# Kernel optimization log

Hardware: AMD Instinct MI355X
Metric: run time of the kernel (lower is better)

The kernel has to match this reference:

```python
import jax, jax.numpy as jnp
import numpy as np

CONFUSED_PAIRS = [(1, 2), (3, 4), (5, 6)]
NUM_CLASSES = 13
MARGIN = 0.5
IGNORE_INDEX = -100
BIG = 1e9  # finite sentinel instead of +/-inf (keeps grads clean)
EPS = 1e-12  # matches F.normalize eps

_conf_np = np.zeros((NUM_CLASSES, NUM_CLASSES), dtype=bool)
for _a, _b in CONFUSED_PAIRS:
    _conf_np[_a, _b] = True
    _conf_np[_b, _a] = True
CONF = jnp.asarray(_conf_np)  # [C, C] symmetric confused-class table


def setup_inputs() -> dict:
    key = jax.random.key(0)
    k1, k2 = jax.random.split(key)
    embeddings = jax.random.normal(k1, (16, 512, 256), dtype=jnp.float32)
    labels = jax.random.randint(k2, (16, 512), 0, 13, dtype=jnp.int64)
    return {"embeddings": embeddings, "labels": labels}


def reference(embeddings, labels):
    B, S, H = embeddings.shape
    e = embeddings.reshape(-1, H)                      # [N, H]
    lab = labels.reshape(-1)                           # [N]
    N = e.shape[0]

    valid = lab != IGNORE_INDEX                        # [N]
    # L2 normalize (F.normalize: divide by norm clamped to eps)
    norm = jnp.linalg.norm(e, axis=1, keepdims=True)
    e = e / jnp.maximum(norm, EPS)

    sim = e @ e.T                                      # [N, N] cosine sims

    lab_c = jnp.clip(lab, 0, NUM_CLASSES - 1)          # safe gather index
    # anchor label participates in some confused pair, and anchor is valid
    anchor_ok = valid & CONF[lab_c].any(axis=1)        # [N]

    same = lab[:, None] == lab[None, :]                # [N, N]
    eye = jnp.eye(N, dtype=bool)
    pos_mask = same & valid[None, :] & ~eye            # positives: same class, not self
    neg_mask = CONF[lab_c[:, None], lab_c[None, :]] & valid[None, :]  # confused-class negatives

    has_pos = pos_mask.any(axis=1)
    has_neg = neg_mask.any(axis=1)
    count_mask = anchor_ok & has_pos & has_neg         # [N] anchors contributing a triplet

    hardest_pos = jnp.min(jnp.where(pos_mask, sim, BIG), axis=1)   # [N]
    hardest_neg = jnp.max(jnp.where(neg_mask, sim, -BIG), axis=1)  # [N]

    triplet = jax.nn.relu(MARGIN + hardest_neg - hardest_pos)
    triplet = jnp.where(count_mask, triplet, 0.0)

    num_triplets = count_mask.sum()
    loss = triplet.sum() / jnp.maximum(num_triplets, 1).astype(triplet.dtype)
    return jnp.where(num_triplets > 0, loss, 0.0)
```

## Files before the change

### kernel.cpp

```cpp
#include <hip/hip_runtime.h>
#include <math.h>

#define Hdim    256
#define NMAX    8192
#define NPADMAX (NMAX + 6 * 32)
#define WLMAX   264
#define BIGV    1e9f
#define MARGIN  0.5f

typedef __attribute__((ext_vector_type(8))) short bf16x8;
typedef __attribute__((ext_vector_type(4))) float f32x4;

struct WS {
    unsigned short ebf[NPADMAX][Hdim];
    int gpos[NMAX];
    int S[8];
    int n[8];
    int wl_a[WLMAX];
    int wl_c[WLMAX];
    int T;
    unsigned done;
    float wsum;
    int   wcnt;
};

__device__ inline unsigned short f2bf(float f) {
    unsigned u = __float_as_uint(f);
    return (unsigned short)((u + 0x7fffu + ((u >> 16) & 1u)) >> 16);
}

__global__ __launch_bounds__(1024) void plan_kernel(const int* __restrict__ lab,
                                                    WS* ws, int N) {
    __shared__ int h[8];
    __shared__ int S[8];
    __shared__ int cur[8];
    const int tid = threadIdx.x;
    if (tid < 8) h[tid] = 0;
    __syncthreads();
    for (int i = tid; i < N; i += 1024) {
        int l = lab[i];
        if (l >= 1 && l <= 6) atomicAdd(&h[l], 1);
    }
    __syncthreads();
    if (tid == 0) {
        int acc = 0;
        for (int c = 1; c <= 6; ++c) { S[c] = acc; acc += ((h[c] + 31) >> 5) << 5; }
        S[0] = 0; S[7] = acc;
        int T = 0;
        for (int c = 1; c <= 6; ++c) {
            int nt = (h[c] + 31) >> 5;
            for (int k = 0; k < nt; ++k) { ws->wl_a[T] = S[c] + 32 * k; ws->wl_c[T] = c; ++T; }
        }
        ws->T = T;
        ws->done = 0u; ws->wsum = 0.f; ws->wcnt = 0;
        for (int c = 0; c < 8; ++c) { ws->n[c] = h[c]; ws->S[c] = S[c]; }
    }
    __syncthreads();
    if (tid < 8) cur[tid] = S[tid];
    __syncthreads();
    for (int i = tid; i < N; i += 1024) {
        int l = lab[i];
        ws->gpos[i] = (l >= 1 && l <= 6) ? atomicAdd(&cur[l], 1) : -1;
    }
}

__global__ __launch_bounds__(256) void norm_gather_kernel(const float* __restrict__ in,
                                                          WS* ws) {
    int row  = blockIdx.x * 4 + (threadIdx.x >> 6);
    int lane = threadIdx.x & 63;
    int g = ws->gpos[row];
    if (g < 0) return;
    float4 v = ((const float4*)(in + (size_t)row * Hdim))[lane];
    float ss = v.x*v.x + v.y*v.y + v.z*v.z + v.w*v.w;
    #pragma unroll
    for (int off = 32; off >= 1; off >>= 1) ss += __shfl_xor(ss, off);
    float sc = 1.0f / fmaxf(sqrtf(ss), 1e-12f);
    ushort4 o;
    o.x = f2bf(v.x * sc); o.y = f2bf(v.y * sc);
    o.z = f2bf(v.z * sc); o.w = f2bf(v.w * sc);
    ((ushort4*)(&ws->ebf[g][0]))[lane] = o;
}

__global__ __launch_bounds__(256) void sim_kernel(WS* ws, float* __restrict__ out) {
    const int wave = threadIdx.x >> 6;
    const int lane = threadIdx.x & 63;
    const int col  = lane & 15;
    const int quad = lane >> 4;
    const int tileIdx = blockIdx.x;

    __shared__ float lds_hp[4][32], lds_hn[4][32];

    if (tileIdx < ws->T) {
        const int aBase = ws->wl_a[tileIdx];
        const int c     = ws->wl_c[tileIdx];
        const int p     = ((c - 1) ^ 1) + 1;
        const int posS = ws->S[c], posRealE = posS + ws->n[c];
        const int negS = ws->S[p], negRealE = negS + ws->n[p];
        const int nPosT = (ws->S[c + 1] - posS) >> 4;
        const int nNegT = (ws->S[p + 1] - negS) >> 4;
        const int nTT   = nPosT + nNegT;
        const bool hasPN = (ws->n[c] >= 2) && (ws->n[p] >= 1);

        const unsigned short* ebf = &ws->ebf[0][0];

        bf16x8 afrag[2][8];
        #pragma unroll
        for (int t2 = 0; t2 < 2; ++t2) {
            const unsigned short* rp = ebf + (size_t)(aBase + t2 * 16 + col) * Hdim + quad * 8;
            #pragma unroll
            for (int ks = 0; ks < 8; ++ks)
                afrag[t2][ks] = *(const bf16x8*)(rp + ks * 32);
        }

        float runMin[2][4], runMax[2][4];
        #pragma unroll
        for (int t2 = 0; t2 < 2; ++t2)
            #pragma unroll
            for (int r = 0; r < 4; ++r) { runMin[t2][r] = BIGV; runMax[t2][r] = -BIGV; }

        auto j0Of = [&](int t) -> int {
            return (t < nPosT) ? (posS + (t << 4)) : (negS + ((t - nPosT) << 4));
        };
        bf16x8 b0[8], b1[8];
        auto loadB = [&](bf16x8 (&bf)[8], int t) {
            const unsigned short* rp = ebf + (size_t)(j0Of(t) + col) * Hdim + quad * 8;
            #pragma unroll
            for (int ks = 0; ks < 8; ++ks)
                bf[ks] = *(const bf16x8*)(rp + ks * 32);
        };
        auto computeT = [&](bf16x8 (&bf)[8], int t) {
            int j0 = j0Of(t);
            bool isPos = t < nPosT;
            int realE  = isPos ? posRealE : negRealE;
            bool valid = (j0 + col) < realE;
            #pragma unroll
            for (int t2 = 0; t2 < 2; ++t2) {
                f32x4 acc = {0.f, 0.f, 0.f, 0.f};
                #pragma unroll
                for (int ks = 0; ks < 8; ++ks)
                    acc = __builtin_amdgcn_mfma_f32_16x16x32_bf16(afrag[t2][ks], bf[ks], acc, 0, 0, 0);
                if (isPos) {
                    #pragma unroll
                    for (int r = 0; r < 4; ++r)
                        runMin[t2][r] = fminf(runMin[t2][r], valid ? acc[r] : BIGV);
                } else {
                    #pragma unroll
                    for (int r = 0; r < 4; ++r)
                        runMax[t2][r] = fmaxf(runMax[t2][r], valid ? acc[r] : -BIGV);
                }
            }
        };

        int nIter = (nTT > wave) ? ((nTT - wave + 3) >> 2) : 0;
        int t = wave, i = 0;
        if (nIter > 0) loadB(b0, t);
        while (i + 2 <= nIter) {
            loadB(b1, t + 4);
            computeT(b0, t);
            if (i + 2 < nIter) loadB(b0, t + 8);
            computeT(b1, t + 4);
            t += 8; i += 2;
        }
        if (i < nIter) computeT(b0, t);

        #pragma unroll
        for (int t2 = 0; t2 < 2; ++t2)
            #pragma unroll
            for (int r = 0; r < 4; ++r) {
                float mn = runMin[t2][r], mx = runMax[t2][r];
                #pragma unroll
                for (int off = 1; off < 16; off <<= 1) {
                    mn = fminf(mn, __shfl_xor(mn, off));
                    mx = fmaxf(mx, __shfl_xor(mx, off));
                }
                if (col == 0) {
                    int a = t2 * 16 + quad * 4 + r;
                    lds_hp[wave][a] = mn;
                    lds_hn[wave][a] = mx;
                }
            }
        __syncthreads();

        if (wave == 0) {
            float contrib = 0.f; int cc = 0;
            if (lane < 32) {
                float hp = fminf(fminf(lds_hp[0][lane], lds_hp[1][lane]),
                                 fminf(lds_hp[2][lane], lds_hp[3][lane]));
                float hn = fmaxf(fmaxf(lds_hn[0][lane], lds_hn[1][lane]),
                                 fmaxf(lds_hn[2][lane], lds_hn[3][lane]));
                bool real = (aBase + lane) < posRealE;
                if (real && hasPN) {
                    float tr = MARGIN + hn - hp;
                    contrib = (tr > 0.f) ? tr : 0.f;
                    cc = 1;
                }
            }
            #pragma unroll
            for (int off = 32; off >= 1; off >>= 1) {
                contrib += __shfl_xor(contrib, off);
                cc      += __shfl_xor(cc, off);
            }
            if (lane == 0) {
                atomicAdd(&ws->wsum, contrib);
                atomicAdd(&ws->wcnt, cc);
            }
        }
    }

    if (threadIdx.x == 0) {
        __builtin_amdgcn_s_waitcnt(0);
        unsigned old = atomicAdd(&ws->done, 1u);
        if (old == (unsigned)(gridDim.x - 1)) {
            float s = atomicAdd(&ws->wsum, 0.0f);
            int   n = atomicAdd(&ws->wcnt, 0);
            out[0] = (n > 0) ? s / (float)n : 0.f;
        }
    }
}

extern "C" void kernel_launch(void* const* d_in, const int* in_sizes, int n_in,
                              void* d_out, int out_size, void* d_ws, size_t ws_size,
                              hipStream_t stream) {
    const float* emb = (const float*)d_in[0];
    const int*   lab = (const int*)d_in[1];
    int N = in_sizes[1];
    WS* ws = (WS*)d_ws;

    plan_kernel<<<1, 1024, 0, stream>>>(lab, ws, N);
    norm_gather_kernel<<<(N + 3) / 4, 256, 0, stream>>>(emb, ws);
    sim_kernel<<<WLMAX, 256, 0, stream>>>(ws, (float*)d_out);
}
```

Before: 94.83 us.

## Merge plan and normalize kernels into one launch with indirection index

Result: slower. 127.5 us (+34.4%).

```diff
diff --git a/kernel.cpp b/kernel.cpp
--- a/kernel.cpp
+++ b/kernel.cpp
@@ -12,8 +12,8 @@
 typedef __attribute__((ext_vector_type(4))) float f32x4;
 
 struct WS {
-    unsigned short ebf[NPADMAX][Hdim];
-    int gpos[NMAX];
+    unsigned short ebf[NMAX][Hdim];
+    int idx[NPADMAX];
     int S[8];
     int n[8];
     int wl_a[WLMAX];
@@ -29,56 +29,90 @@
     return (unsigned short)((u + 0x7fffu + ((u >> 16) & 1u)) >> 16);
 }
 
-__global__ __launch_bounds__(1024) void plan_kernel(const int* __restrict__ lab,
-                                                    WS* ws, int N) {
-    __shared__ int h[8];
-    __shared__ int S[8];
-    __shared__ int cur[8];
-    const int tid = threadIdx.x;
-    if (tid < 8) h[tid] = 0;
-    __syncthreads();
-    for (int i = tid; i < N; i += 1024) {
-        int l = lab[i];
-        if (l >= 1 && l <= 6) atomicAdd(&h[l], 1);
+__global__ __launch_bounds__(256) void prep_kernel(const float* __restrict__ in,
+                                                   const int* __restrict__ lab,
+                                                   WS* ws, int N) {
+    if (blockIdx.x == 0) {
+        __shared__ int h[8], S[8], cur[8], ntp[8];
+        const int tid  = threadIdx.x;
+        const int lane = tid & 63;
+        const int wv   = tid >> 6;
+        if (tid < 8) h[tid] = 0;
+        __syncthreads();
+
+        int cnt[7] = {0, 0, 0, 0, 0, 0, 0};
+        for (int base = wv * 64; base < N; base += 256) {
+            int l = lab[base + lane];
+            #pragma unroll
+            for (int c = 1; c <= 6; ++c)
+                cnt[c] += (int)__popcll(__ballot(l == c));
+        }
+        if (lane == 0) {
+            #pragma unroll
+            for (int c = 1; c <= 6; ++c) atomicAdd(&h[c], cnt[c]);
+        }
+        __syncthreads();
+
+        if (tid == 0) {
+            int acc = 0, tt = 0;
+            #pragma unroll
+            for (int c = 1; c <= 6; ++c) {
+                S[c]   = acc; acc += ((h[c] + 31) >> 5) << 5;
+                ntp[c] = tt;  tt  += (h[c] + 31) >> 5;
+            }
+            S[0] = 0; S[7] = acc; ntp[0] = 0; ntp[7] = tt;
+            ws->T = tt;
+            ws->done = 0u; ws->wsum = 0.f; ws->wcnt = 0;
+            #pragma unroll
+            for (int c = 0; c < 8; ++c) { ws->n[c] = h[c]; ws->S[c] = S[c]; }
+        }
+        __syncthreads();
+
+        if (tid < 8) cur[tid] = S[tid];
+        if (tid < ntp[7]) {
+            int c = 1;
+            while (tid >= ntp[c + 1]) ++c;
+            ws->wl_a[tid] = S[c] + ((tid - ntp[c]) << 5);
+            ws->wl_c[tid] = c;
+        }
+        if (tid < 192) {
+            int c = (tid >> 5) + 1;
+            int s = S[c] + h[c] + (tid & 31);
+            if (s < S[c + 1]) ws->idx[s] = 0;
+        }
+        __syncthreads();
+
+        for (int base = wv * 64; base < N; base += 256) {
+            int i = base + lane;
+            int l = lab[i];
+            #pragma unroll
+            for (int c = 1; c <= 6; ++c) {
+                unsigned long long m = __ballot(l == c);
+                if (m != 0ull) {
+                    int ldr = (int)__ffsll((unsigned long long)m) - 1;
+                    int b = 0;
+                    if (lane == ldr) b = atomicAdd(&cur[c], (int)__popcll(m));
+                    b = __shfl(b, ldr);
+                    if (l == c)
+                        ws->idx[b + (int)__popcll(m & ((1ull << lane) - 1ull))] = i;
+                }
+            }
+        }
+    } else {
+        const int row  = (blockIdx.x - 1) * 4 + (threadIdx.x >> 6);
+        const int lane = threadIdx.x & 63;
+        const int l = lab[row];
+        if (l < 1 || l > 6) return;
+        float4 v = ((const float4*)(in + (size_t)row * Hdim))[lane];
+        float ss = v.x*v.x + v.y*v.y + v.z*v.z + v.w*v.w;
+        #pragma unroll
+        for (int off = 32; off >= 1; off >>= 1) ss += __shfl_xor(ss, off);
+        float sc = 1.0f / fmaxf(sqrtf(ss), 1e-12f);
+        ushort4 o;
+        o.x = f2bf(v.x * sc); o.y = f2bf(v.y * sc);
+        o.z = f2bf(v.z * sc); o.w = f2bf(v.w * sc);
+        ((ushort4*)(&ws->ebf[row][0]))[lane] = o;
     }
-    __syncthreads();
-    if (tid == 0) {
-        int acc = 0;
-        for (int c = 1; c <= 6; ++c) { S[c] = acc; acc += ((h[c] + 31) >> 5) << 5; }
-        S[0] = 0; S[7] = acc;
-        int T = 0;
-        for (int c = 1; c <= 6; ++c) {
-            int nt = (h[c] + 31) >> 5;
-            for (int k = 0; k < nt; ++k) { ws->wl_a[T] = S[c] + 32 * k; ws->wl_c[T] = c; ++T; }
-        }
-        ws->T = T;
-        ws->done = 0u; ws->wsum = 0.f; ws->wcnt = 0;
-        for (int c = 0; c < 8; ++c) { ws->n[c] = h[c]; ws->S[c] = S[c]; }
-    }
-    __syncthreads();
-    if (tid < 8) cur[tid] = S[tid];
-    __syncthreads();
-    for (int i = tid; i < N; i += 1024) {
-        int l = lab[i];
-        ws->gpos[i] = (l >= 1 && l <= 6) ? atomicAdd(&cur[l], 1) : -1;
-    }
-}
-
-__global__ __launch_bounds__(256) void norm_gather_kernel(const float* __restrict__ in,
-                                                          WS* ws) {
-    int row  = blockIdx.x * 4 + (threadIdx.x >> 6);
-    int lane = threadIdx.x & 63;
-    int g = ws->gpos[row];
-    if (g < 0) return;
-    float4 v = ((const float4*)(in + (size_t)row * Hdim))[lane];
-    float ss = v.x*v.x + v.y*v.y + v.z*v.z + v.w*v.w;
-    #pragma unroll
-    for (int off = 32; off >= 1; off >>= 1) ss += __shfl_xor(ss, off);
-    float sc = 1.0f / fmaxf(sqrtf(ss), 1e-12f);
-    ushort4 o;
-    o.x = f2bf(v.x * sc); o.y = f2bf(v.y * sc);
-    o.z = f2bf(v.z * sc); o.w = f2bf(v.w * sc);
-    ((ushort4*)(&ws->ebf[g][0]))[lane] = o;
 }
 
 __global__ __launch_bounds__(256) void sim_kernel(WS* ws, float* __restrict__ out) {
@@ -102,11 +136,13 @@
         const bool hasPN = (ws->n[c] >= 2) && (ws->n[p] >= 1);
 
         const unsigned short* ebf = &ws->ebf[0][0];
+        const int* __restrict__ idx = ws->idx;
 
         bf16x8 afrag[2][8];
         #pragma unroll
         for (int t2 = 0; t2 < 2; ++t2) {
-            const unsigned short* rp = ebf + (size_t)(aBase + t2 * 16 + col) * Hdim + quad * 8;
+            int ar = idx[aBase + t2 * 16 + col];
+            const unsigned short* rp = ebf + (size_t)ar * Hdim + quad * 8;
             #pragma unroll
             for (int ks = 0; ks < 8; ++ks)
                 afrag[t2][ks] = *(const bf16x8*)(rp + ks * 32);
@@ -123,7 +159,8 @@
         };
         bf16x8 b0[8], b1[8];
         auto loadB = [&](bf16x8 (&bf)[8], int t) {
-            const unsigned short* rp = ebf + (size_t)(j0Of(t) + col) * Hdim + quad * 8;
+            int jr = idx[j0Of(t) + col];
+            const unsigned short* rp = ebf + (size_t)jr * Hdim + quad * 8;
             #pragma unroll
             for (int ks = 0; ks < 8; ++ks)
                 bf[ks] = *(const bf16x8*)(rp + ks * 32);
@@ -226,7 +263,6 @@
     int N = in_sizes[1];
     WS* ws = (WS*)d_ws;
 
-    plan_kernel<<<1, 1024, 0, stream>>>(lab, ws, N);
-    norm_gather_kernel<<<(N + 3) / 4, 256, 0, stream>>>(emb, ws);
+    prep_kernel<<<1 + (N + 3) / 4, 256, 0, stream>>>(emb, lab, ws, N);
     sim_kernel<<<WLMAX, 256, 0, stream>>>(ws, (float*)d_out);
 }
```
